# Performance work log

Hardware: AMD Instinct MI355X
Metric: run time of the kernel (lower is better)

Reference implementation:

```python
import jax, jax.numpy as jnp
import numpy as np

BN_EPS = 1e-5
CLUSTER_SIZE = 32  # K (real clusters kept after softmax)


def setup_inputs() -> dict:
    key = jax.random.key(0)
    ks = jax.random.split(key, 7)
    B, N, D, Ktot, K = 4096, 128, 512, 48, 32
    x = jax.random.normal(ks[0], (B, N, D), dtype=jnp.float32)
    clusters = jax.random.normal(ks[1], (D, Ktot), dtype=jnp.float32) / np.sqrt(D)
    bn_w = jax.random.uniform(ks[2], (Ktot,), dtype=jnp.float32)
    bn_b = jax.random.normal(ks[3], (Ktot,), dtype=jnp.float32)
    bn_rm = jax.random.normal(ks[4], (Ktot,), dtype=jnp.float32)
    bn_rv = jax.random.uniform(ks[5], (Ktot,), dtype=jnp.float32)  # positive variance
    clusters2 = jax.random.normal(ks[6], (1, D, K), dtype=jnp.float32) / np.sqrt(D)
    return {"x": x, "clusters": clusters, "bn_w": bn_w, "bn_b": bn_b,
            "bn_rm": bn_rm, "bn_rv": bn_rv, "clusters2": clusters2}


def reference(x, clusters, bn_w, bn_b, bn_rm, bn_rv, clusters2):
    # x: [B, N, D]; clusters: [D, Ktot]; clusters2: [1, D, K]
    B, N, D = x.shape
    K = clusters2.shape[-1]
    # cluster projection: [B, N, Ktot]
    logits = jnp.einsum('bnd,dk->bnk', x, clusters)
    # inference BatchNorm1d (affine with running stats)
    inv_std = jax.lax.rsqrt(bn_rv + BN_EPS)
    logits = (logits - bn_rm) * inv_std * bn_w + bn_b
    # softmax over real + ghost clusters, then drop ghost (no renorm)
    assignment = jax.nn.softmax(logits, axis=-1)[..., :K]  # [B, N, K]
    a_sum = jnp.sum(assignment, axis=1, keepdims=True)      # [B, 1, K]
    a = a_sum * clusters2                                   # [B, D, K]
    # weighted VLAD accumulate: [B, D, K]
    vlad = jnp.einsum('bnk,bnd->bdk', assignment, x) - a
    # intra-normalize (L2 across descriptor dim D, per cluster)
    vlad = vlad / jnp.maximum(jnp.linalg.norm(vlad, axis=1, keepdims=True), 1e-12)
    # flatten and L2-normalize full vector
    vlad = vlad.reshape(B, D * K)
    vlad = vlad / jnp.maximum(jnp.linalg.norm(vlad, axis=1, keepdims=True), 1e-12)
    return vlad
```

## Files before the change

### kernel.cpp

```cpp
#include <hip/hip_runtime.h>

typedef unsigned short u16;
typedef unsigned int u32;
typedef __attribute__((ext_vector_type(8))) short short8;
typedef __attribute__((ext_vector_type(4))) float f32x4;
typedef __attribute__((ext_vector_type(4))) u32 u32x4;

#define NPT 128
#define DIM 512
#define KT 48
#define KC 32
#define BPB 16

__device__ __forceinline__ u16 f2bf(float f) {
    unsigned u = __builtin_bit_cast(unsigned, f);
    return (u16)((u + 0x7FFFu + ((u >> 16) & 1u)) >> 16);
}

__device__ __forceinline__ u32 cvtpk(float lo, float hi) {
    u32 r;
    asm("v_cvt_pk_bf16_f32 %0, %1, %2" : "=v"(r) : "v"(lo), "v"(hi));
    return r;
}

__device__ __forceinline__ void lds_barrier() {
    asm volatile("s_waitcnt lgkmcnt(0)" ::: "memory");
    __builtin_amdgcn_s_barrier();
}

__device__ __forceinline__ int swz(int n) {
    return ((n & 7) ^ ((n >> 3) & 7)) << 4;
}

__global__ void prep_kernel(const float* __restrict__ clusters,
                            const float* __restrict__ bn_w,
                            const float* __restrict__ bn_b,
                            const float* __restrict__ bn_rm,
                            const float* __restrict__ bn_rv,
                            u16* __restrict__ cTs,
                            float* __restrict__ tvec) {
    const int k = blockIdx.x;
    const float s = bn_w[k] * rsqrtf(bn_rv[k] + 1e-5f);
    if (threadIdx.x == 0) tvec[k] = bn_b[k] - bn_rm[k] * s;
    for (int d = threadIdx.x; d < DIM; d += blockDim.x)
        cTs[k * DIM + d] = f2bf(clusters[d * KT + k] * s);
}

__global__ __launch_bounds__(512)
void vlad_kernel(const float* __restrict__ x,
                 const float* __restrict__ c2,
                 const u16* __restrict__ cTs,
                 const float* __restrict__ tvec,
                 float* __restrict__ out) {
    __shared__ __align__(16) u16 cTsL[KT * DIM];
    __shared__ __align__(16) u16 buf[2][16 * DIM];
    __shared__ __align__(16) u16 aT[KC][136];
    __shared__ float asum_part[8][KC];
    __shared__ float colsq_part[8][KC];

    const int tid  = threadIdx.x;
    const int wave = tid >> 6;
    const int lane = tid & 63;
    const int lr   = lane & 15;
    const int lg   = lane >> 4;

    const int b0i = blockIdx.x * BPB;
    const float* xblk = x + (size_t)b0i * (NPT * DIM);

    const float t0 = tvec[lr], t1 = tvec[16 + lr], t2 = tvec[32 + lr];

    const int srow = tid >> 5;
    const int scol = (tid & 31) * 16;
    const int sbyte = scol * 2;
    const int ssw = swz(srow);

    #pragma unroll
    for (int i = 0; i < 6; ++i) {
        int idx = tid + i * 512;
        int k = idx >> 6, slot = idx & 63;
        u32x4 v = *(const u32x4*)(cTs + k * DIM + slot * 8);
        *(u32x4*)((char*)cTsL + k * 1024 + ((slot * 16) ^ swz(k))) = v;
    }
    {
        const float* g = xblk + srow * DIM + scol;
        f32x4 a0 = *(const f32x4*)(g);
        f32x4 a1 = *(const f32x4*)(g + 4);
        f32x4 a2 = *(const f32x4*)(g + 8);
        f32x4 a3 = *(const f32x4*)(g + 12);
        u32x4 wA, wB;
        wA[0] = cvtpk(a0[0], a0[1]); wA[1] = cvtpk(a0[2], a0[3]);
        wA[2] = cvtpk(a1[0], a1[1]); wA[3] = cvtpk(a1[2], a1[3]);
        wB[0] = cvtpk(a2[0], a2[1]); wB[1] = cvtpk(a2[2], a2[3]);
        wB[2] = cvtpk(a3[0], a3[1]); wB[3] = cvtpk(a3[2], a3[3]);
        char* dst = (char*)buf[0] + srow * 1024;
        *(u32x4*)(dst + (sbyte ^ ssw)) = wA;
        *(u32x4*)(dst + ((sbyte + 16) ^ ssw)) = wB;
    }
    __syncthreads();

    for (int m = 0; m < BPB; ++m) {
        f32x4 acc0 = {0.f,0.f,0.f,0.f}, acc1 = {0.f,0.f,0.f,0.f}, acc2 = {0.f,0.f,0.f,0.f};
        short8 af2[4][4];

        #pragma unroll
        for (int ns = 0; ns < 4; ++ns) {
            #pragma unroll
            for (int h = 0; h < 2; ++h) {
                const int j = ns * 2 + h;
                const int cur = j & 1;
                const int gnext = m * 8 + j + 1;
                const bool pOK = (gnext < BPB * 8);

                f32x4 a0, a1, a2, a3;
                if (pOK) {
                    const float* g = xblk + (size_t)gnext * (16 * DIM) + srow * DIM + scol;
                    a0 = *(const f32x4*)(g);
                    a1 = *(const f32x4*)(g + 4);
                    a2 = *(const f32x4*)(g + 8);
                    a3 = *(const f32x4*)(g + 12);
                }

                if ((lane >> 5) == h) {
                    const int nb = (lg & 1) * 8;
                    #pragma unroll
                    for (int dti = 0; dti < 4; ++dti) {
                        const int dd = wave * 128 + dti * 32 + 2 * lr;
                        short8 v;
                        #pragma unroll
                        for (int jj = 0; jj < 8; ++jj) {
                            const int rr = nb + jj;
                            v[jj] = *(const short*)((const char*)buf[cur] + rr * 1024 + (dd ^ swz(rr)));
                        }
                        af2[ns][dti] = v;
                    }
                }

                if (wave == j) {
                    const char* xb = (const char*)buf[cur] + lr * 1024;
                    const int sw = swz(lr);
                    const char* c0 = (const char*)cTsL + lr * 1024;
                    const char* c1 = (const char*)cTsL + (16 + lr) * 1024;
                    const char* c2p = (const char*)cTsL + (32 + lr) * 1024;
                    const int s1 = swz(16 + lr), s2 = swz(32 + lr);
                    #pragma unroll 2
                    for (int step = 0; step < 16; ++step) {
                        const int off = step * 64 + lg * 16;
                        short8 af  = *(const short8*)(xb + (off ^ sw));
                        short8 bb0 = *(const short8*)(c0 + (off ^ sw));
                        short8 bb1 = *(const short8*)(c1 + (off ^ s1));
                        short8 bb2 = *(const short8*)(c2p + (off ^ s2));
                        acc0 = __builtin_amdgcn_mfma_f32_16x16x32_bf16(af, bb0, acc0, 0, 0, 0);
                        acc1 = __builtin_amdgcn_mfma_f32_16x16x32_bf16(af, bb1, acc1, 0, 0, 0);
                        acc2 = __builtin_amdgcn_mfma_f32_16x16x32_bf16(af, bb2, acc2, 0, 0, 0);
                    }
                }

                if (pOK) {
                    u32x4 wA, wB;
                    wA[0] = cvtpk(a0[0], a0[1]); wA[1] = cvtpk(a0[2], a0[3]);
                    wA[2] = cvtpk(a1[0], a1[1]); wA[3] = cvtpk(a1[2], a1[3]);
                    wB[0] = cvtpk(a2[0], a2[1]); wB[1] = cvtpk(a2[2], a2[3]);
                    wB[2] = cvtpk(a3[0], a3[1]); wB[3] = cvtpk(a3[2], a3[3]);
                    char* dst = (char*)buf[cur ^ 1] + srow * 1024;
                    *(u32x4*)(dst + (sbyte ^ ssw)) = wA;
                    *(u32x4*)(dst + ((sbyte + 16) ^ ssw)) = wB;
                }
                lds_barrier();
            }
        }

        {
            float a0[4], a1[4];
            #pragma unroll
            for (int r = 0; r < 4; ++r) {
                float l0 = acc0[r] + t0, l1 = acc1[r] + t1, l2 = acc2[r] + t2;
                float mx = fmaxf(fmaxf(l0, l1), l2);
                #pragma unroll
                for (int o = 1; o < 16; o <<= 1) mx = fmaxf(mx, __shfl_xor(mx, o));
                float e0 = __expf(l0 - mx), e1 = __expf(l1 - mx), e2 = __expf(l2 - mx);
                float s = e0 + e1 + e2;
                #pragma unroll
                for (int o = 1; o < 16; o <<= 1) s += __shfl_xor(s, o);
                float inv = 1.0f / s;
                a0[r] = e0 * inv; a1[r] = e1 * inv;
            }
            float p0 = 0.f, p1 = 0.f;
            #pragma unroll
            for (int r = 0; r < 4; ++r) {
                int n = wave * 16 + lg * 4 + r;
                aT[lr][n]      = f2bf(a0[r]);
                aT[16 + lr][n] = f2bf(a1[r]);
                p0 += a0[r]; p1 += a1[r];
            }
            p0 += __shfl_xor(p0, 16); p0 += __shfl_xor(p0, 32);
            p1 += __shfl_xor(p1, 16); p1 += __shfl_xor(p1, 32);
            if (lane < 16) { asum_part[wave][lane] = p0; asum_part[wave][16 + lane] = p1; }
        }
        lds_barrier();

        f32x4 vacc[4][2];
        #pragma unroll
        for (int i = 0; i < 4; ++i) {
            vacc[i][0] = (f32x4){0.f,0.f,0.f,0.f};
            vacc[i][1] = (f32x4){0.f,0.f,0.f,0.f};
        }
        #pragma unroll
        for (int ns = 0; ns < 4; ++ns) {
            short8 bf0 = *(const short8*)(&aT[lr][ns * 32 + lg * 8]);
            short8 bf1 = *(const short8*)(&aT[16 + lr][ns * 32 + lg * 8]);
            #pragma unroll
            for (int dti = 0; dti < 4; ++dti) {
                vacc[dti][0] = __builtin_amdgcn_mfma_f32_16x16x32_bf16(af2[ns][dti], bf0, vacc[dti][0], 0, 0, 0);
                vacc[dti][1] = __builtin_amdgcn_mfma_f32_16x16x32_bf16(af2[ns][dti], bf1, vacc[dti][1], 0, 0, 0);
            }
        }

        float as0 = 0.f, as1 = 0.f;
        #pragma unroll
        for (int w2 = 0; w2 < 8; ++w2) {
            as0 += asum_part[w2][lr];
            as1 += asum_part[w2][16 + lr];
        }
        float cs0 = 0.f, cs1 = 0.f;
        #pragma unroll
        for (int dti = 0; dti < 4; ++dti) {
            #pragma unroll
            for (int r = 0; r < 4; ++r) {
                int d = (wave * 4 + dti) * 16 + lg * 4 + r;
                float v0 = vacc[dti][0][r] - as0 * c2[d * KC + lr];
                float v1 = vacc[dti][1][r] - as1 * c2[d * KC + 16 + lr];
                vacc[dti][0][r] = v0; vacc[dti][1][r] = v1;
                cs0 += v0 * v0; cs1 += v1 * v1;
            }
        }
        cs0 += __shfl_xor(cs0, 16); cs0 += __shfl_xor(cs0, 32);
        cs1 += __shfl_xor(cs1, 16); cs1 += __shfl_xor(cs1, 32);
        if (lane < 16) { colsq_part[wave][lane] = cs0; colsq_part[wave][16 + lane] = cs1; }
        lds_barrier();
        float sq0 = 0.f, sq1 = 0.f;
        #pragma unroll
        for (int w2 = 0; w2 < 8; ++w2) {
            sq0 += colsq_part[w2][lr];
            sq1 += colsq_part[w2][16 + lr];
        }
        float cn0 = sqrtf(sq0), cn1 = sqrtf(sq1);
        float s10 = 1.0f / fmaxf(cn0, 1e-12f);
        float s11 = 1.0f / fmaxf(cn1, 1e-12f);
        float c10 = cn0 * s10, c11 = cn1 * s11;
        float tot = c10 * c10 + c11 * c11;
        #pragma unroll
        for (int o = 1; o < 16; o <<= 1) tot += __shfl_xor(tot, o);
        float gs = 1.0f / fmaxf(sqrtf(tot), 1e-12f);
        float sk0 = s10 * gs, sk1 = s11 * gs;
        {
            float* ob = out + (size_t)(b0i + m) * (DIM * KC);
            #pragma unroll
            for (int dti = 0; dti < 4; ++dti) {
                #pragma unroll
                for (int r = 0; r < 4; ++r) {
                    int d = (wave * 4 + dti) * 16 + lg * 4 + r;
                    ob[d * KC + lr]      = vacc[dti][0][r] * sk0;
                    ob[d * KC + 16 + lr] = vacc[dti][1][r] * sk1;
                }
            }
        }
    }
}

extern "C" void kernel_launch(void* const* d_in, const int* in_sizes, int n_in,
                              void* d_out, int out_size, void* d_ws, size_t ws_size,
                              hipStream_t stream) {
    const float* x        = (const float*)d_in[0];
    const float* clusters = (const float*)d_in[1];
    const float* bn_w     = (const float*)d_in[2];
    const float* bn_b     = (const float*)d_in[3];
    const float* bn_rm    = (const float*)d_in[4];
    const float* bn_rv    = (const float*)d_in[5];
    const float* c2       = (const float*)d_in[6];
    float* out = (float*)d_out;

    u16*   cTs  = (u16*)d_ws;
    float* tvec = (float*)((char*)d_ws + KT * DIM * sizeof(u16));

    const int B = in_sizes[0] / (NPT * DIM);

    prep_kernel<<<KT, 256, 0, stream>>>(clusters, bn_w, bn_b, bn_rm, bn_rv, cTs, tvec);
    vlad_kernel<<<B / BPB, 512, 0, stream>>>(x, c2, cTs, tvec, out);
}
```

Baseline: 368.3 us.

## Stage 32-row x chunks with two-deep register prefetch and fewer barriers

```diff
diff --git a/kernel.cpp b/kernel.cpp
--- a/kernel.cpp
+++ b/kernel.cpp
@@ -11,6 +11,7 @@
 #define KT 48
 #define KC 32
 #define BPB 16
+#define NCH (BPB * 4)
 
 __device__ __forceinline__ u16 f2bf(float f) {
     unsigned u = __builtin_bit_cast(unsigned, f);
@@ -46,6 +47,40 @@
         cTs[k * DIM + d] = f2bf(clusters[d * KT + k] * s);
 }
 
+#define Z_ISSUE(c)                                                           \
+    do {                                                                     \
+        const float* gp_ = xblk + (size_t)(c) * (32 * DIM);                  \
+        _Pragma("unroll")                                                    \
+        for (int p = 0; p < 2; ++p) {                                        \
+            const float* q_ = gp_ + (srow + 16 * p) * DIM + scol;            \
+            z[p][0] = *(const f32x4*)(q_);                                   \
+            z[p][1] = *(const f32x4*)(q_ + 4);                               \
+            z[p][2] = *(const f32x4*)(q_ + 8);                               \
+            z[p][3] = *(const f32x4*)(q_ + 12);                              \
+        }                                                                    \
+    } while (0)
+
+#define Z_WRITE(bufp)                                                        \
+    do {                                                                     \
+        _Pragma("unroll")                                                    \
+        for (int p = 0; p < 2; ++p) {                                        \
+            const int r_ = srow + 16 * p;                                    \
+            const int sw_ = swz(r_);                                         \
+            u32x4 wA, wB;                                                    \
+            wA[0] = cvtpk(z[p][0][0], z[p][0][1]);                           \
+            wA[1] = cvtpk(z[p][0][2], z[p][0][3]);                           \
+            wA[2] = cvtpk(z[p][1][0], z[p][1][1]);                           \
+            wA[3] = cvtpk(z[p][1][2], z[p][1][3]);                           \
+            wB[0] = cvtpk(z[p][2][0], z[p][2][1]);                           \
+            wB[1] = cvtpk(z[p][2][2], z[p][2][3]);                           \
+            wB[2] = cvtpk(z[p][3][0], z[p][3][1]);                           \
+            wB[3] = cvtpk(z[p][3][2], z[p][3][3]);                           \
+            char* dst_ = (char*)(bufp) + r_ * 1024;                          \
+            *(u32x4*)(dst_ + (sbyte ^ sw_)) = wA;                            \
+            *(u32x4*)(dst_ + ((sbyte + 16) ^ sw_)) = wB;                     \
+        }                                                                    \
+    } while (0)
+
 __global__ __launch_bounds__(512)
 void vlad_kernel(const float* __restrict__ x,
                  const float* __restrict__ c2,
@@ -53,7 +88,7 @@
                  const float* __restrict__ tvec,
                  float* __restrict__ out) {
     __shared__ __align__(16) u16 cTsL[KT * DIM];
-    __shared__ __align__(16) u16 buf[2][16 * DIM];
+    __shared__ __align__(16) u16 buf[2][32 * DIM];
     __shared__ __align__(16) u16 aT[KC][136];
     __shared__ float asum_part[8][KC];
     __shared__ float colsq_part[8][KC];
@@ -72,7 +107,8 @@
     const int srow = tid >> 5;
     const int scol = (tid & 31) * 16;
     const int sbyte = scol * 2;
-    const int ssw = swz(srow);
+
+    f32x4 z[2][4];
 
     #pragma unroll
     for (int i = 0; i < 6; ++i) {
@@ -81,21 +117,9 @@
         u32x4 v = *(const u32x4*)(cTs + k * DIM + slot * 8);
         *(u32x4*)((char*)cTsL + k * 1024 + ((slot * 16) ^ swz(k))) = v;
     }
-    {
-        const float* g = xblk + srow * DIM + scol;
-        f32x4 a0 = *(const f32x4*)(g);
-        f32x4 a1 = *(const f32x4*)(g + 4);
-        f32x4 a2 = *(const f32x4*)(g + 8);
-        f32x4 a3 = *(const f32x4*)(g + 12);
-        u32x4 wA, wB;
-        wA[0] = cvtpk(a0[0], a0[1]); wA[1] = cvtpk(a0[2], a0[3]);
-        wA[2] = cvtpk(a1[0], a1[1]); wA[3] = cvtpk(a1[2], a1[3]);
-        wB[0] = cvtpk(a2[0], a2[1]); wB[1] = cvtpk(a2[2], a2[3]);
-        wB[2] = cvtpk(a3[0], a3[1]); wB[3] = cvtpk(a3[2], a3[3]);
-        char* dst = (char*)buf[0] + srow * 1024;
-        *(u32x4*)(dst + (sbyte ^ ssw)) = wA;
-        *(u32x4*)(dst + ((sbyte + 16) ^ ssw)) = wB;
-    }
+    Z_ISSUE(0);
+    Z_WRITE(buf[0]);
+    Z_ISSUE(1);
     __syncthreads();
 
     for (int m = 0; m < BPB; ++m) {
@@ -103,70 +127,50 @@
         short8 af2[4][4];
 
         #pragma unroll
-        for (int ns = 0; ns < 4; ++ns) {
-            #pragma unroll
-            for (int h = 0; h < 2; ++h) {
-                const int j = ns * 2 + h;
-                const int cur = j & 1;
-                const int gnext = m * 8 + j + 1;
-                const bool pOK = (gnext < BPB * 8);
-
-                f32x4 a0, a1, a2, a3;
-                if (pOK) {
-                    const float* g = xblk + (size_t)gnext * (16 * DIM) + srow * DIM + scol;
-                    a0 = *(const f32x4*)(g);
-                    a1 = *(const f32x4*)(g + 4);
-                    a2 = *(const f32x4*)(g + 8);
-                    a3 = *(const f32x4*)(g + 12);
+        for (int j = 0; j < 4; ++j) {
+            const int g = m * 4 + j;
+            const int cur = j & 1;
+
+            {
+                const int nb = lg * 8;
+                #pragma unroll
+                for (int dti = 0; dti < 4; ++dti) {
+                    const int dd = wave * 128 + dti * 32 + 2 * lr;
+                    short8 v;
+                    #pragma unroll
+                    for (int jj = 0; jj < 8; ++jj) {
+                        const int rr = nb + jj;
+                        v[jj] = *(const short*)((const char*)buf[cur] + rr * 1024 + (dd ^ swz(rr)));
+                    }
+                    af2[j][dti] = v;
                 }
-
-                if ((lane >> 5) == h) {
-                    const int nb = (lg & 1) * 8;
-                    #pragma unroll
-                    for (int dti = 0; dti < 4; ++dti) {
-                        const int dd = wave * 128 + dti * 32 + 2 * lr;
-                        short8 v;
-                        #pragma unroll
-                        for (int jj = 0; jj < 8; ++jj) {
-                            const int rr = nb + jj;
-                            v[jj] = *(const short*)((const char*)buf[cur] + rr * 1024 + (dd ^ swz(rr)));
-                        }
-                        af2[ns][dti] = v;
-                    }
+            }
+
+            if ((wave >> 1) == j) {
+                const int cr = (wave & 1) * 16 + lr;
+                const char* xb = (const char*)buf[cur] + cr * 1024;
+                const int swx = swz(cr);
+                const char* cb0 = (const char*)cTsL + lr * 1024;
+                const char* cb1 = (const char*)cTsL + (16 + lr) * 1024;
+                const char* cb2 = (const char*)cTsL + (32 + lr) * 1024;
+                const int s0 = swz(lr), s1 = swz(16 + lr), s2 = swz(32 + lr);
+                #pragma unroll 2
+                for (int step = 0; step < 16; ++step) {
+                    const int off = step * 64 + lg * 16;
+                    short8 af  = *(const short8*)(xb  + (off ^ swx));
+                    short8 bb0 = *(const short8*)(cb0 + (off ^ s0));
+                    short8 bb1 = *(const short8*)(cb1 + (off ^ s1));
+                    short8 bb2 = *(const short8*)(cb2 + (off ^ s2));
+                    acc0 = __builtin_amdgcn_mfma_f32_16x16x32_bf16(af, bb0, acc0, 0, 0, 0);
+                    acc1 = __builtin_amdgcn_mfma_f32_16x16x32_bf16(af, bb1, acc1, 0, 0, 0);
+                    acc2 = __builtin_amdgcn_mfma_f32_16x16x32_bf16(af, bb2, acc2, 0, 0, 0);
                 }
-
-                if (wave == j) {
-                    const char* xb = (const char*)buf[cur] + lr * 1024;
-                    const int sw = swz(lr);
-                    const char* c0 = (const char*)cTsL + lr * 1024;
-                    const char* c1 = (const char*)cTsL + (16 + lr) * 1024;
-                    const char* c2p = (const char*)cTsL + (32 + lr) * 1024;
-                    const int s1 = swz(16 + lr), s2 = swz(32 + lr);
-                    #pragma unroll 2
-                    for (int step = 0; step < 16; ++step) {
-                        const int off = step * 64 + lg * 16;
-                        short8 af  = *(const short8*)(xb + (off ^ sw));
-                        short8 bb0 = *(const short8*)(c0 + (off ^ sw));
-                        short8 bb1 = *(const short8*)(c1 + (off ^ s1));
-                        short8 bb2 = *(const short8*)(c2p + (off ^ s2));
-                        acc0 = __builtin_amdgcn_mfma_f32_16x16x32_bf16(af, bb0, acc0, 0, 0, 0);
-                        acc1 = __builtin_amdgcn_mfma_f32_16x16x32_bf16(af, bb1, acc1, 0, 0, 0);
-                        acc2 = __builtin_amdgcn_mfma_f32_16x16x32_bf16(af, bb2, acc2, 0, 0, 0);
-                    }
-                }
-
-                if (pOK) {
-                    u32x4 wA, wB;
-                    wA[0] = cvtpk(a0[0], a0[1]); wA[1] = cvtpk(a0[2], a0[3]);
-                    wA[2] = cvtpk(a1[0], a1[1]); wA[3] = cvtpk(a1[2], a1[3]);
-                    wB[0] = cvtpk(a2[0], a2[1]); wB[1] = cvtpk(a2[2], a2[3]);
-                    wB[2] = cvtpk(a3[0], a3[1]); wB[3] = cvtpk(a3[2], a3[3]);
-                    char* dst = (char*)buf[cur ^ 1] + srow * 1024;
-                    *(u32x4*)(dst + (sbyte ^ ssw)) = wA;
-                    *(u32x4*)(dst + ((sbyte + 16) ^ ssw)) = wB;
-                }
-                lds_barrier();
-            }
+            }
+
+            if (g + 1 < NCH) { Z_WRITE(buf[cur ^ 1]); }
+            if (j < 3 && g + 2 < NCH) { Z_ISSUE(g + 2); }
+
+            lds_barrier();
         }
 
         {
@@ -264,6 +268,8 @@
                 }
             }
         }
+
+        if (m + 1 < BPB) { Z_ISSUE((m + 1) * 4 + 1); }
     }
 }
 
```

Result: slower. 403.9 us (+9.7%).
